# Performance work log

Measured on AMD Instinct MI355X. Metric: run time of the kernel, lower is better.

The kernel has to match this reference:

```python
import jax, jax.numpy as jnp
import numpy as np
from jax import lax

EPS = 1e-5
IC = 32  # inter_channels

def bn(x, g, b, m, v):
    sh = (1, -1, 1, 1)
    return (x - m.reshape(sh)) * (g.reshape(sh) * lax.rsqrt(v.reshape(sh) + EPS)) + b.reshape(sh)

def prelu(x, a):
    return jnp.where(x >= 0, x, a * x)

def conv1x1(x, w):  # x: [B,C,H,W], w: [O,C]
    return jnp.einsum('bchw,oc->bohw', x, w)

def dconv(x, w, d):  # 3x3 dilated conv, same padding
    return lax.conv_general_dilated(x, w, (1, 1), [(d, d), (d, d)], rhs_dilation=(d, d),
                                    dimension_numbers=('NCHW', 'OIHW', 'NCHW'))

def glca_forward(feature, q_w, q_gamma, q_beta, q_mean, q_var, q_alpha,
                 k_w, k_gamma, k_beta, k_mean, k_var, k_alpha,
                 v_w, v_gamma, v_beta, v_mean, v_var, v_alpha,
                 d1_w, d1_gamma, d1_beta, d1_mean, d1_var,
                 d2_w, d2_gamma, d2_beta, d2_mean, d2_var,
                 d3_w, d3_gamma, d3_beta, d3_mean, d3_var,
                 o_w, o_gamma, o_beta, o_mean, o_var, o_alpha):
    B, C, H, W = feature.shape
    q = prelu(bn(conv1x1(feature, q_w), q_gamma, q_beta, q_mean, q_var), q_alpha)  # [B,IC,H,W]
    k = prelu(bn(conv1x1(feature, k_w), k_gamma, k_beta, k_mean, k_var), k_alpha)
    val = prelu(bn(conv1x1(feature, v_w), v_gamma, v_beta, v_mean, v_var), v_alpha)
    qr = q.transpose(0, 3, 2, 1).reshape(B * W, H, IC)   # [BW,H,IC]
    kr = k.transpose(0, 3, 1, 2).reshape(B * W, IC, H)   # [BW,IC,H]
    att = jax.nn.softmax(jnp.matmul(qr, kr), axis=-1)    # [BW,H,H]
    branches = []
    for w, g, b, m, var, d in ((d1_w, d1_gamma, d1_beta, d1_mean, d1_var, 1),
                               (d2_w, d2_gamma, d2_beta, d2_mean, d2_var, 3),
                               (d3_w, d3_gamma, d3_beta, d3_mean, d3_var, 5)):
        t = jax.nn.relu(bn(dconv(val, w, d), g, b, m, var))          # [B,IC,H,W]
        # faithful to source: permute(0,3,1,2) then raw view to [BW,H,IC]
        t = t.transpose(0, 3, 1, 2).reshape(B * W, H, IC)
        branches.append(jnp.matmul(att, t))                          # [BW,H,IC]
    # faithful to source: cat along dim 0, then raw view(B,W,H,-1)
    res = jnp.concatenate(branches, axis=0).reshape(B, W, H, 3 * IC)
    res = res.transpose(0, 3, 2, 1)                                  # [B,3*IC,H,W]
    out = prelu(bn(conv1x1(res, o_w), o_gamma, o_beta, o_mean, o_var) + feature, o_alpha)
    return out

def setup_inputs() -> dict:
    B, C, H, W = 8, 256, 160, 160
    key = jax.random.key(0)
    ks = iter(jax.random.split(key, 48))
    d = {}
    d['feature'] = jax.random.normal(next(ks), (B, C, H, W), jnp.float32)
    for p in ('q', 'k', 'v'):
        d[p + '_w'] = jax.random.normal(next(ks), (IC, C), jnp.float32) * 0.05
        d[p + '_gamma'] = jax.random.uniform(next(ks), (IC,), jnp.float32, 0.5, 1.5)
        d[p + '_beta'] = jax.random.normal(next(ks), (IC,), jnp.float32) * 0.1
        d[p + '_mean'] = jax.random.normal(next(ks), (IC,), jnp.float32) * 0.1
        d[p + '_var'] = jax.random.uniform(next(ks), (IC,), jnp.float32, 0.5, 1.5)
        d[p + '_alpha'] = jnp.full((1,), 0.25, jnp.float32)
    for p in ('d1', 'd2', 'd3'):
        d[p + '_w'] = jax.random.normal(next(ks), (IC, IC, 3, 3), jnp.float32) * 0.05
        d[p + '_gamma'] = jax.random.uniform(next(ks), (IC,), jnp.float32, 0.5, 1.5)
        d[p + '_beta'] = jax.random.normal(next(ks), (IC,), jnp.float32) * 0.1
        d[p + '_mean'] = jax.random.normal(next(ks), (IC,), jnp.float32) * 0.1
        d[p + '_var'] = jax.random.uniform(next(ks), (IC,), jnp.float32, 0.5, 1.5)
    d['o_w'] = jax.random.normal(next(ks), (C, 3 * IC), jnp.float32) * 0.05
    d['o_gamma'] = jax.random.uniform(next(ks), (C,), jnp.float32, 0.5, 1.5)
    d['o_beta'] = jax.random.normal(next(ks), (C,), jnp.float32) * 0.1
    d['o_mean'] = jax.random.normal(next(ks), (C,), jnp.float32) * 0.1
    d['o_var'] = jax.random.uniform(next(ks), (C,), jnp.float32, 0.5, 1.5)
    d['o_alpha'] = jnp.full((1,), 0.25, jnp.float32)
    return d

def reference(feature, q_w, q_gamma, q_beta, q_mean, q_var, q_alpha,
              k_w, k_gamma, k_beta, k_mean, k_var, k_alpha,
              v_w, v_gamma, v_beta, v_mean, v_var, v_alpha,
              d1_w, d1_gamma, d1_beta, d1_mean, d1_var,
              d2_w, d2_gamma, d2_beta, d2_mean, d2_var,
              d3_w, d3_gamma, d3_beta, d3_mean, d3_var,
              o_w, o_gamma, o_beta, o_mean, o_var, o_alpha):
    return glca_forward(feature, q_w, q_gamma, q_beta, q_mean, q_var, q_alpha,
                        k_w, k_gamma, k_beta, k_mean, k_var, k_alpha,
                        v_w, v_gamma, v_beta, v_mean, v_var, v_alpha,
                        d1_w, d1_gamma, d1_beta, d1_mean, d1_var,
                        d2_w, d2_gamma, d2_beta, d2_mean, d2_var,
                        d3_w, d3_gamma, d3_beta, d3_mean, d3_var,
                        o_w, o_gamma, o_beta, o_mean, o_var, o_alpha)
```

## Files before the change

kernel.cpp:

```cpp
#include <hip/hip_runtime.h>

constexpr int Hh = 160, Ww = 160, Bb = 8, Cc = 256, ICn = 32;
constexpr int HWn = Hh * Ww;
constexpr float EPSf = 1e-5f;

constexpr int P_WQH  = 0;
constexpr int P_WQL  = 12288;
constexpr int P_QKVB = 24576;
constexpr int P_QKVA = 24672;
constexpr int P_DWB  = 24768;
constexpr int P_DB   = 52416;
constexpr int P_OWB  = 52512;
constexpr int P_OB   = 77088;
constexpr int P_OA   = 77344;
constexpr int PLANE  = Bb * ICn * HWn;
constexpr int OFF_Q  = 77824;
constexpr int OFF_K  = OFF_Q + PLANE;
constexpr int OFF_V  = OFF_Q + 2 * PLANE;
constexpr int OFF_T  = OFF_Q + 3 * PLANE;
constexpr int OFF_TPF= OFF_T + (3 * PLANE) / 2;
constexpr int OFF_CAT= OFF_Q + 6 * PLANE;

typedef unsigned short u16;
typedef short bf16x8 __attribute__((ext_vector_type(8)));
typedef float f32x4  __attribute__((ext_vector_type(4)));

__device__ __forceinline__ unsigned f2b(float x) {
    unsigned u = __float_as_uint(x);
    return (u + 0x7FFFu + ((u >> 16) & 1u)) >> 16;
}
__device__ __forceinline__ float b2f(unsigned b) { return __uint_as_float(b << 16); }

struct InPtrs { const float* p[40]; };

__global__ void k_prep(InPtrs in, float* __restrict__ ws) {
    int idx = blockIdx.x * 256 + threadIdx.x;
    if (idx < 24576) {
        int oc = idx >> 8, c = idx & 255;
        int z = oc >> 5, o = oc & 31;
        const float* wz = in.p[1 + 6 * z];
        float s = in.p[2 + 6 * z][o] * rsqrtf(in.p[5 + 6 * z][o] + EPSf);
        float wf = wz[o * 256 + c] * s;
        unsigned hi = f2b(wf);
        unsigned lo = f2b(wf - b2f(hi));
        ((u16*)(ws + P_WQH))[oc * 256 + c] = (u16)hi;
        ((u16*)(ws + P_WQL))[oc * 256 + c] = (u16)lo;
    } else if (idx < 24672) {
        int oc = idx - 24576; int z = oc >> 5, o = oc & 31;
        float s = in.p[2 + 6 * z][o] * rsqrtf(in.p[5 + 6 * z][o] + EPSf);
        ws[P_QKVB + oc] = in.p[3 + 6 * z][o] - in.p[4 + 6 * z][o] * s;
    } else if (idx < 24768) {
        int oc = idx - 24672; int z = oc >> 5;
        ws[P_QKVA + oc] = in.p[6 + 6 * z][0];
    } else if (idx < 52416) {
        int j = idx - 24768;
        int d = j / 9216, r2 = j % 9216;
        int oc = r2 & 31; int tmp = r2 >> 5;
        int kx = tmp % 3; tmp /= 3; int ky = tmp % 3; int ic2 = tmp / 3;
        const float* wd = in.p[19 + 5 * d];
        float s = in.p[20 + 5 * d][oc] * rsqrtf(in.p[23 + 5 * d][oc] + EPSf);
        float wf = wd[((oc * 32 + ic2) * 3 + ky) * 3 + kx] * s;
        ((u16*)(ws + P_DWB))[((d * 9 + ky * 3 + kx) * 32 + oc) * 32 + ic2] = (u16)f2b(wf);
    } else if (idx < 52512) {
        int j = idx - 52416; int d = j >> 5, oc = j & 31;
        float s = in.p[20 + 5 * d][oc] * rsqrtf(in.p[23 + 5 * d][oc] + EPSf);
        ws[P_DB + j] = in.p[21 + 5 * d][oc] - in.p[22 + 5 * d][oc] * s;
    } else if (idx < 77088) {
        int j2 = idx - 52512; int c = j2 / 96;
        float s = in.p[35][c] * rsqrtf(in.p[38][c] + EPSf);
        ((u16*)(ws + P_OWB))[j2] = (u16)f2b(in.p[34][j2] * s);
    } else if (idx < 77344) {
        int c = idx - 77088;
        float s = in.p[35][c] * rsqrtf(in.p[38][c] + EPSf);
        ws[P_OB + c] = in.p[36][c] - in.p[37][c] * s;
    } else if (idx == 77344) {
        ws[P_OA] = in.p[39][0];
    }
}

__global__ __launch_bounds__(64) void k_vpad(float* __restrict__ ws) {
    u16* Vt = (u16*)(ws + OFF_V);
    size_t base = (size_t)blockIdx.x * 176 * 32;
    int t = threadIdx.x;
    int off = (t < 32) ? t * 8 : (168 * 32 + (t - 32) * 8);
    uint4 z = {0u, 0u, 0u, 0u};
    *(uint4*)(Vt + base + off) = z;
}

__global__ __launch_bounds__(256) void k_qkv(const float* __restrict__ feat,
                                             float* __restrict__ ws) {
    __shared__ float FS[64 * 132];
    const int tid = threadIdx.x;
    const int wv = tid >> 6, l = tid & 63;
    const int g = l >> 4, c15 = l & 15;
    const int n0 = blockIdx.x * 128;
    const int b = n0 / HWn, hw0 = n0 % HWn;
    const float* fbase = feat + (size_t)b * Cc * HWn + hw0;
    const u16* __restrict__ WQH = (const u16*)(ws + P_WQH);
    const u16* __restrict__ WQL = (const u16*)(ws + P_WQL);

    f32x4 acc[6][2];
    f32x4 z4 = {0.f, 0.f, 0.f, 0.f};
#pragma unroll
    for (int mt = 0; mt < 6; mt++) { acc[mt][0] = z4; acc[mt][1] = z4; }

    for (int kc = 0; kc < 4; kc++) {
        __syncthreads();
#pragma unroll
        for (int i = 0; i < 8; i++) {
            int f = tid + i * 256;
            int row = f >> 5, col4 = f & 31;
            float4 v = *(const float4*)(fbase + (size_t)(kc * 64 + row) * HWn + col4 * 4);
            *(float4*)(&FS[row * 132 + col4 * 4]) = v;
        }
        __syncthreads();
#pragma unroll
        for (int ks = 0; ks < 2; ks++) {
            bf16x8 bh[2], bl[2];
#pragma unroll
            for (int ntl = 0; ntl < 2; ntl++) {
                int pos = (wv * 2 + ntl) * 16 + c15;
                unsigned hw_[4], lw_[4];
#pragma unroll
                for (int v2 = 0; v2 < 4; v2++) {
                    float x0 = FS[(ks * 32 + g * 8 + 2 * v2) * 132 + pos];
                    float x1 = FS[(ks * 32 + g * 8 + 2 * v2 + 1) * 132 + pos];
                    unsigned h0 = f2b(x0), h1 = f2b(x1);
                    unsigned l0 = f2b(x0 - b2f(h0)), l1 = f2b(x1 - b2f(h1));
                    hw_[v2] = h0 | (h1 << 16);
                    lw_[v2] = l0 | (l1 << 16);
                }
                uint4 hv = {hw_[0], hw_[1], hw_[2], hw_[3]};
                uint4 lv = {lw_[0], lw_[1], lw_[2], lw_[3]};
                bh[ntl] = *(bf16x8*)&hv;
                bl[ntl] = *(bf16x8*)&lv;
            }
#pragma unroll
            for (int mt = 0; mt < 6; mt++) {
                int arow = (16 * mt + c15) * 256 + kc * 64 + ks * 32 + g * 8;
                bf16x8 ah = *(const bf16x8*)(WQH + arow);
                bf16x8 al = *(const bf16x8*)(WQL + arow);
#pragma unroll
                for (int ntl = 0; ntl < 2; ntl++) {
                    acc[mt][ntl] = __builtin_amdgcn_mfma_f32_16x16x32_bf16(ah, bh[ntl], acc[mt][ntl], 0, 0, 0);
                    acc[mt][ntl] = __builtin_amdgcn_mfma_f32_16x16x32_bf16(ah, bl[ntl], acc[mt][ntl], 0, 0, 0);
                    acc[mt][ntl] = __builtin_amdgcn_mfma_f32_16x16x32_bf16(al, bh[ntl], acc[mt][ntl], 0, 0, 0);
                }
            }
        }
    }

    u16* vt = (u16*)(ws + OFF_V);
#pragma unroll
    for (int mt = 0; mt < 6; mt++)
#pragma unroll
        for (int ntl = 0; ntl < 2; ntl++) {
            int pos = hw0 + (wv * 2 + ntl) * 16 + c15;
            if (mt < 4) {
#pragma unroll
                for (int jr = 0; jr < 4; jr++) {
                    int oc = 16 * mt + 4 * g + jr;
                    float bb = ws[P_QKVB + oc];
                    float aa = ws[P_QKVA + oc];
                    float y = acc[mt][ntl][jr] + bb;
                    y = y >= 0.f ? y : aa * y;
                    int z = oc >> 5, o = oc & 31;
                    ws[OFF_Q + (size_t)z * PLANE + ((size_t)b * ICn + o) * HWn + pos] = y;
                }
            } else {
                int h = pos / 160, w2 = pos % 160;
                unsigned r[2];
#pragma unroll
                for (int p = 0; p < 2; p++) {
                    int oc = 16 * mt + 4 * g + 2 * p;
                    float y0 = acc[mt][ntl][2 * p]     + ws[P_QKVB + oc];
                    float y1 = acc[mt][ntl][2 * p + 1] + ws[P_QKVB + oc + 1];
                    float a0 = ws[P_QKVA + oc], a1 = ws[P_QKVA + oc + 1];
                    y0 = y0 >= 0.f ? y0 : a0 * y0;
                    y1 = y1 >= 0.f ? y1 : a1 * y1;
                    r[p] = f2b(y0) | (f2b(y1) << 16);
                }
                size_t a = ((size_t)(b * 160 + h) * 176 + w2 + 8) * 32 + (mt - 4) * 16 + 4 * g;
                uint2 dd; dd.x = r[0]; dd.y = r[1];
                *(uint2*)(vt + a) = dd;
            }
        }
}

__global__ __launch_bounds__(256) void k_dconv(float* __restrict__ ws) {
    const int tid = threadIdx.x;
    const int wv = tid >> 6, l = tid & 63;
    const int g = l >> 4, c15 = l & 15;
    const int b = blockIdx.y;
    const int d = blockIdx.z;
    const int dil = 1 + 2 * d;
    const int h0 = blockIdx.x * 2;
    const u16* __restrict__ WB = (const u16*)(ws + P_DWB) + d * 9 * 32 * 32;
    bf16x8 wb[9][2];
#pragma unroll
    for (int tap = 0; tap < 9; tap++)
#pragma unroll
        for (int n = 0; n < 2; n++)
            wb[tap][n] = *(const bf16x8*)(WB + ((size_t)tap * 32 + n * 16 + c15) * 32 + g * 8);
    const u16* __restrict__ Vt = (const u16*)(ws + OFF_V) + (size_t)b * 160 * 176 * 32;
    const float bias0 = ws[P_DB + d * 32 + c15];
    const float bias1 = ws[P_DB + d * 32 + 16 + c15];
    u16* __restrict__ tp = (u16*)(ws + OFF_TPF) + (size_t)(d * Bb + b) * ICn * HWn;
    f32x4 z4 = {0.f, 0.f, 0.f, 0.f};

    for (int t5 = 0; t5 < 5; t5++) {
        int t = wv * 5 + t5;
        int h = h0 + (t >= 10);
        int w0 = (t % 10) * 16;
        f32x4 acc0 = z4, acc1 = z4;
#pragma unroll
        for (int ky = 0; ky < 3; ky++) {
            int hh = h + dil * (ky - 1);
            if ((unsigned)hh >= 160u) continue;
            const u16* row = Vt + (size_t)hh * 176 * 32;
#pragma unroll
            for (int kx = 0; kx < 3; kx++) {
                int wbase = w0 + dil * (kx - 1) + 8;
                bf16x8 av = *(const bf16x8*)(row + (size_t)(wbase + c15) * 32 + g * 8);
                acc0 = __builtin_amdgcn_mfma_f32_16x16x32_bf16(av, wb[ky * 3 + kx][0], acc0, 0, 0, 0);
                acc1 = __builtin_amdgcn_mfma_f32_16x16x32_bf16(av, wb[ky * 3 + kx][1], acc1, 0, 0, 0);
            }
        }
        size_t pixb = (size_t)h * 160 + w0 + 4 * g;
        uint2 o0, o1;
        o0.x = f2b(fmaxf(acc0[0] + bias0, 0.f)) | (f2b(fmaxf(acc0[1] + bias0, 0.f)) << 16);
        o0.y = f2b(fmaxf(acc0[2] + bias0, 0.f)) | (f2b(fmaxf(acc0[3] + bias0, 0.f)) << 16);
        o1.x = f2b(fmaxf(acc1[0] + bias1, 0.f)) | (f2b(fmaxf(acc1[1] + bias1, 0.f)) << 16);
        o1.y = f2b(fmaxf(acc1[2] + bias1, 0.f)) | (f2b(fmaxf(acc1[3] + bias1, 0.f)) << 16);
        *(uint2*)(tp + (size_t)c15 * HWn + pixb) = o0;
        *(uint2*)(tp + (size_t)(16 + c15) * HWn + pixb) = o1;
    }
}

__global__ __launch_bounds__(256) void k_tfrag(float* __restrict__ ws) {
    __shared__ u16 fr[4][5120];
    const int tid = threadIdx.x;
    const int wq = blockIdx.x;
    const int b  = blockIdx.y;
    const int d  = blockIdx.z;
    const int w0 = wq * 4;
    const u16* __restrict__ tp = (const u16*)(ws + OFF_TPF) + (size_t)(d * Bb + b) * ICn * HWn;
    for (int i = tid; i < 5120; i += 256) {
        int ic = i / 160, h = i % 160;
        uint2 v = *(const uint2*)(tp + (size_t)ic * HWn + h * Ww + w0);
        fr[0][i] = (u16)(v.x & 0xFFFFu);
        fr[1][i] = (u16)(v.x >> 16);
        fr[2][i] = (u16)(v.y & 0xFFFFu);
        fr[3][i] = (u16)(v.y >> 16);
    }
    __syncthreads();
    u16* __restrict__ tf = (u16*)(ws + OFF_T);
#pragma unroll
    for (int it = 0; it < 10; it++) {
        int W = tid + it * 256;
        int s = W / 640, word = W % 640;
        int slot = word >> 6, lane = word & 63;
        int jc = (lane & 15) | ((slot / 5) << 4);
        int h2b = ((slot % 5) << 5) | (((lane >> 4) & 3) << 3);
        unsigned r[4];
#pragma unroll
        for (int p = 0; p < 4; p++) {
            int f0 = (h2b + 2 * p) * 32 + jc;
            unsigned lo = fr[s][f0];
            unsigned hi = fr[s][f0 + 32];
            r[p] = lo | (hi << 16);
        }
        uint4 o4 = {r[0], r[1], r[2], r[3]};
        *(uint4*)(tf + ((size_t)d * 1280 + b * 160 + w0 + s) * 5120 + word * 8) = o4;
    }
}

__global__ __launch_bounds__(256) void k_qkfrag(float* __restrict__ ws) {
    extern __shared__ float frf[];
    const int tid = threadIdx.x;
    const int wq = blockIdx.x;
    const int b  = blockIdx.y;
    const int z  = blockIdx.z;
    const int w0 = wq * 4;
    const float* __restrict__ in = ws + (z ? OFF_K : OFF_Q) + (size_t)b * ICn * HWn;
    u16* __restrict__ outb = (u16*)(ws + (z ? OFF_TPF : OFF_V));

    for (int i = tid; i < 5120; i += 256) {
        int ic = i / 160, h = i % 160;
        float4 v = *(const float4*)(in + (size_t)ic * HWn + h * 160 + w0);
        frf[0 * 5120 + i] = v.x;
        frf[1 * 5120 + i] = v.y;
        frf[2 * 5120 + i] = v.z;
        frf[3 * 5120 + i] = v.w;
    }
    __syncthreads();
#pragma unroll
    for (int it = 0; it < 10; it++) {
        int W = tid + it * 256;
        int s = W / 640, word = W % 640;
        int lane = word & 63, tau = word >> 6;
        int h = tau * 16 + (lane & 15);
        int icb = (lane >> 4) * 8;
        unsigned hw_[4], lw_[4];
#pragma unroll
        for (int p = 0; p < 4; p++) {
            float x0 = frf[s * 5120 + (icb + 2 * p) * 160 + h];
            float x1 = frf[s * 5120 + (icb + 2 * p + 1) * 160 + h];
            unsigned h0 = f2b(x0), h1 = f2b(x1);
            unsigned l0 = f2b(x0 - b2f(h0)), l1 = f2b(x1 - b2f(h1));
            hw_[p] = h0 | (h1 << 16);
            lw_[p] = l0 | (l1 << 16);
        }
        uint4 hv = {hw_[0], hw_[1], hw_[2], hw_[3]};
        uint4 lv = {lw_[0], lw_[1], lw_[2], lw_[3]};
        size_t o = (size_t)(b * 160 + w0 + s) * 5120 + word * 8;
        *(uint4*)(outb + o) = hv;
        *(uint4*)(outb + (size_t)PLANE + o) = lv;
    }
}

__global__ __launch_bounds__(320) void k_att(float* __restrict__ ws) {
    __shared__ char Sb[51200];
    const int tid = threadIdx.x;
    const int bid = blockIdx.x;
    const int r8 = bid & 7, qq = bid >> 3;
    const int b = qq / 20;
    const int w = r8 * 20 + (qq % 20);
    const int bw = b * Ww + w;
    const int wv = tid >> 6;
    const int l  = tid & 63;
    const int g  = l >> 4;
    const int c  = l & 15;
    const int slice = b * 160 + w;

    const u16* __restrict__ qh = (const u16*)(ws + OFF_V)   + (size_t)slice * 5120;
    const u16* __restrict__ ql = qh + (size_t)PLANE;
    const u16* __restrict__ kh = (const u16*)(ws + OFF_TPF) + (size_t)slice * 5120;
    const u16* __restrict__ kl = kh + (size_t)PLANE;

    bf16x8 bq[2][2];
#pragma unroll
    for (int ct = 0; ct < 2; ct++) {
        int tau = 2 * wv + ct;
        bq[ct][0] = *(const bf16x8*)(qh + (tau * 64 + l) * 8);
        bq[ct][1] = *(const bf16x8*)(ql + (tau * 64 + l) * 8);
    }
    f32x4 acc[10][2];
    f32x4 z4 = {0.f, 0.f, 0.f, 0.f};
#pragma unroll
    for (int rt = 0; rt < 10; rt++) { acc[rt][0] = z4; acc[rt][1] = z4; }
#pragma unroll
    for (int rt = 0; rt < 10; rt++) {
        bf16x8 ah = *(const bf16x8*)(kh + (rt * 64 + l) * 8);
        bf16x8 al = *(const bf16x8*)(kl + (rt * 64 + l) * 8);
#pragma unroll
        for (int ct = 0; ct < 2; ct++) {
            acc[rt][ct] = __builtin_amdgcn_mfma_f32_16x16x32_bf16(ah, bq[ct][0], acc[rt][ct], 0, 0, 0);
            acc[rt][ct] = __builtin_amdgcn_mfma_f32_16x16x32_bf16(ah, bq[ct][1], acc[rt][ct], 0, 0, 0);
            acc[rt][ct] = __builtin_amdgcn_mfma_f32_16x16x32_bf16(al, bq[ct][0], acc[rt][ct], 0, 0, 0);
        }
    }

    float mx[2] = {-3.4e38f, -3.4e38f};
#pragma unroll
    for (int rt = 0; rt < 10; rt++)
#pragma unroll
        for (int ct = 0; ct < 2; ct++)
#pragma unroll
            for (int j = 0; j < 4; j++) mx[ct] = fmaxf(mx[ct], acc[rt][ct][j]);
#pragma unroll
    for (int ct = 0; ct < 2; ct++) {
        mx[ct] = fmaxf(mx[ct], __shfl_xor(mx[ct], 16));
        mx[ct] = fmaxf(mx[ct], __shfl_xor(mx[ct], 32));
    }
    float sm[2] = {0.f, 0.f};
#pragma unroll
    for (int rt = 0; rt < 10; rt++)
#pragma unroll
        for (int ct = 0; ct < 2; ct++)
#pragma unroll
            for (int j = 0; j < 4; j++) {
                float e = __expf(acc[rt][ct][j] - mx[ct]);
                acc[rt][ct][j] = e;
                sm[ct] += e;
            }
#pragma unroll
    for (int ct = 0; ct < 2; ct++) {
        sm[ct] += __shfl_xor(sm[ct], 16);
        sm[ct] += __shfl_xor(sm[ct], 32);
    }
    float inv[2] = {1.f / sm[0], 1.f / sm[1]};

#pragma unroll
    for (int rt = 0; rt < 10; rt++) {
#pragma unroll
        for (int ct = 0; ct < 2; ct++) {
            float p0 = acc[rt][ct][0] * inv[ct];
            float p1 = acc[rt][ct][1] * inv[ct];
            float p2 = acc[rt][ct][2] * inv[ct];
            float p3 = acc[rt][ct][3] * inv[ct];
            unsigned d0 = f2b(p0) | (f2b(p1) << 16);
            unsigned d1 = f2b(p2) | (f2b(p3) << 16);
            int Lf = c + 16 * (2 * (rt & 1) + (g >> 1));
            char* dst = Sb + (((wv * 2 + ct) * 5 + (rt >> 1)) * 64 + Lf) * 16 + 8 * (g & 1);
            uint2 dd; dd.x = d0; dd.y = d1;
            *(uint2*)dst = dd;
        }
    }

    const u16* tf = (const u16*)(ws + OFF_T);
    u16* catb = (u16*)(ws + OFF_CAT);
    for (int d = 0; d < 3; d++) {
        const u16* tfd = tf + ((size_t)d * (Bb * Ww) + bw) * 5120;
        f32x4 po[2][2];
        po[0][0] = z4; po[0][1] = z4; po[1][0] = z4; po[1][1] = z4;
#pragma unroll
        for (int ks = 0; ks < 5; ks++) {
            bf16x8 a0 = *(const bf16x8*)(tfd + ((0 * 5 + ks) * 64 + l) * 8);
            bf16x8 a1 = *(const bf16x8*)(tfd + ((1 * 5 + ks) * 64 + l) * 8);
            bf16x8 s0 = *(bf16x8*)(Sb + (((wv * 2 + 0) * 5 + ks) * 64 + l) * 16);
            bf16x8 s1 = *(bf16x8*)(Sb + (((wv * 2 + 1) * 5 + ks) * 64 + l) * 16);
            po[0][0] = __builtin_amdgcn_mfma_f32_16x16x32_bf16(a0, s0, po[0][0], 0, 0, 0);
            po[0][1] = __builtin_amdgcn_mfma_f32_16x16x32_bf16(a0, s1, po[0][1], 0, 0, 0);
            po[1][0] = __builtin_amdgcn_mfma_f32_16x16x32_bf16(a1, s0, po[1][0], 0, 0, 0);
            po[1][1] = __builtin_amdgcn_mfma_f32_16x16x32_bf16(a1, s1, po[1][1], 0, 0, 0);
        }
#pragma unroll
        for (int jt = 0; jt < 2; jt++)
#pragma unroll
            for (int ct = 0; ct < 2; ct++) {
                int h1 = 32 * wv + 16 * ct + c;
                size_t idx = (size_t)d * PLANE + (size_t)bw * 5120 + h1 * 32 + 16 * jt + 4 * g;
                f32x4 v = po[jt][ct];
                uint2 dd;
                dd.x = f2b(v[0]) | (f2b(v[1]) << 16);
                dd.y = f2b(v[2]) | (f2b(v[3]) << 16);
                *(uint2*)(catb + idx) = dd;
            }
    }
}

__global__ __launch_bounds__(256) void k_out(const float* __restrict__ feat,
                                             const float* __restrict__ ws,
                                             float* __restrict__ out) {
    __shared__ u16 Bs[12288];
    const int tid = threadIdx.x;
    const int wv = tid >> 6, l = tid & 63;
    const int g = l >> 4, c15 = l & 15;
    const int n0 = blockIdx.x * 128;
    const int b = n0 / HWn, hw0 = n0 % HWn;
    const u16* __restrict__ CATb = (const u16*)(ws + OFF_CAT);
    const u16* __restrict__ OWB = (const u16*)(ws + P_OWB);

#pragma unroll
    for (int ss = 0; ss < 6; ss++) {
        int s = tid + ss * 256;
        int sl = s & 63, si = s >> 6;
        int p = (si & 7) * 16 + (sl & 15);
        int hw = hw0 + p;
        int h = hw / Ww, w2 = hw % Ww;
        int j = (si >> 3) * 32 + (sl >> 4) * 8;
        size_t flat = ((size_t)(b * Ww + w2) * Hh + h) * 96 + j;
        *(uint4*)(&Bs[(si * 64 + sl) * 8]) = *(const uint4*)(CATb + flat);
    }
    bf16x8 af[4][3];
#pragma unroll
    for (int mt = 0; mt < 4; mt++)
#pragma unroll
        for (int ks = 0; ks < 3; ks++)
            af[mt][ks] = *(const bf16x8*)(OWB + (wv * 64 + mt * 16 + c15) * 96 + ks * 32 + g * 8);
    __syncthreads();
    const float alpha = ws[P_OA];

    f32x4 z4 = {0.f, 0.f, 0.f, 0.f};
#pragma unroll
    for (int np = 0; np < 2; np++) {
        f32x4 acc[4][4];
#pragma unroll
        for (int mt = 0; mt < 4; mt++)
#pragma unroll
            for (int ntl = 0; ntl < 4; ntl++) acc[mt][ntl] = z4;
#pragma unroll
        for (int ks = 0; ks < 3; ks++) {
            bf16x8 bf_[4];
#pragma unroll
            for (int ntl = 0; ntl < 4; ntl++)
                bf_[ntl] = *(const bf16x8*)(&Bs[((ks * 8 + np * 4 + ntl) * 64 + l) * 8]);
#pragma unroll
            for (int mt = 0; mt < 4; mt++)
#pragma unroll
                for (int ntl = 0; ntl < 4; ntl++)
                    acc[mt][ntl] = __builtin_amdgcn_mfma_f32_16x16x32_bf16(af[mt][ks], bf_[ntl], acc[mt][ntl], 0, 0, 0);
        }
#pragma unroll
        for (int mt = 0; mt < 4; mt++)
#pragma unroll
            for (int ntl = 0; ntl < 4; ntl++) {
                int p = (np * 4 + ntl) * 16 + c15;
#pragma unroll
                for (int jr = 0; jr < 4; jr++) {
                    int cch = wv * 64 + mt * 16 + 4 * g + jr;
                    size_t base = ((size_t)b * Cc + cch) * HWn + hw0 + p;
                    float y = acc[mt][ntl][jr] + ws[P_OB + cch] + feat[base];
                    out[base] = y >= 0.f ? y : alpha * y;
                }
            }
    }
}

extern "C" void kernel_launch(void* const* d_in, const int* in_sizes, int n_in,
                              void* d_out, int out_size, void* d_ws, size_t ws_size,
                              hipStream_t stream) {
    InPtrs ip;
    for (int i = 0; i < 40; i++) ip.p[i] = (const float*)d_in[i];
    float* ws = (float*)d_ws;
    const float* feat = (const float*)d_in[0];
    float* out = (float*)d_out;

    k_prep<<<304, 256, 0, stream>>>(ip, ws);
    k_vpad<<<1280, 64, 0, stream>>>(ws);
    k_qkv<<<1600, 256, 0, stream>>>(feat, ws);
    k_dconv<<<dim3(80, 8, 3), 256, 0, stream>>>(ws);
    k_tfrag<<<dim3(40, 8, 3), 256, 0, stream>>>(ws);
    (void)hipFuncSetAttribute(reinterpret_cast<const void*>(k_qkfrag),
                              hipFuncAttributeMaxDynamicSharedMemorySize, 81920);
    k_qkfrag<<<dim3(40, 8, 2), 256, 81920, stream>>>(ws);
    k_att<<<1280, 320, 0, stream>>>(ws);
    k_out<<<1600, 256, 0, stream>>>(feat, ws, out);
}
```

Before: 471.2 us.

## Pipeline k_qkv feature loads with async global-to-LDS four-stage ring buffer

Replaces the synchronous register-staged load of feature tiles in the QKV projection kernel with direct global-to-LDS async loads into a 4-deep ring of 32-channel slices, gated by explicit vmcnt waits and barriers. Loads for later chunks are issued while MFMA work runs on earlier ones, to hide global memory latency. LDS use grows to 64 KB of dynamic shared memory, which may lower occupancy. The LDS row padding is removed, so bank conflicts on reads may rise.

```diff
diff --git a/kernel.cpp b/kernel.cpp
--- a/kernel.cpp
+++ b/kernel.cpp
@@ -30,6 +30,10 @@
     return (u + 0x7FFFu + ((u >> 16) & 1u)) >> 16;
 }
 __device__ __forceinline__ float b2f(unsigned b) { return __uint_as_float(b << 16); }
+
+#define GLOAD_LDS16(gp, lp) __builtin_amdgcn_global_load_lds( \
+    (const __attribute__((address_space(1))) void*)(gp), \
+    (__attribute__((address_space(3))) void*)(lp), 16, 0, 0)
 
 struct InPtrs { const float* p[40]; };
 
@@ -89,7 +93,7 @@
 
 __global__ __launch_bounds__(256) void k_qkv(const float* __restrict__ feat,
                                              float* __restrict__ ws) {
-    __shared__ float FS[64 * 132];
+    extern __shared__ float FSs[];
     const int tid = threadIdx.x;
     const int wv = tid >> 6, l = tid & 63;
     const int g = l >> 4, c15 = l & 15;
@@ -104,49 +108,63 @@
 #pragma unroll
     for (int mt = 0; mt < 6; mt++) { acc[mt][0] = z4; acc[mt][1] = z4; }
 
+#pragma unroll
     for (int kc = 0; kc < 4; kc++) {
-        __syncthreads();
-#pragma unroll
-        for (int i = 0; i < 8; i++) {
-            int f = tid + i * 256;
-            int row = f >> 5, col4 = f & 31;
-            float4 v = *(const float4*)(fbase + (size_t)(kc * 64 + row) * HWn + col4 * 4);
-            *(float4*)(&FS[row * 132 + col4 * 4]) = v;
-        }
-        __syncthreads();
-#pragma unroll
-        for (int ks = 0; ks < 2; ks++) {
-            bf16x8 bh[2], bl[2];
+        float* dst = FSs + kc * 4096 + wv * 1024;
+        const float* src = fbase + (size_t)(kc * 32 + wv * 8) * HWn;
+#pragma unroll
+        for (int j = 0; j < 4; j++)
+            GLOAD_LDS16(src + (size_t)(2 * j + (l >> 5)) * HWn + (l & 31) * 4, dst + j * 256);
+    }
+
+#pragma unroll
+    for (int kc = 0; kc < 8; kc++) {
+        if (kc <= 4)      asm volatile("s_waitcnt vmcnt(12)" ::: "memory");
+        else if (kc == 5) asm volatile("s_waitcnt vmcnt(8)" ::: "memory");
+        else if (kc == 6) asm volatile("s_waitcnt vmcnt(4)" ::: "memory");
+        else              asm volatile("s_waitcnt vmcnt(0)" ::: "memory");
+        __builtin_amdgcn_s_barrier();
+        asm volatile("" ::: "memory");
+        const float* B = FSs + (kc & 3) * 4096;
+        bf16x8 bh[2], bl[2];
+#pragma unroll
+        for (int ntl = 0; ntl < 2; ntl++) {
+            int pos = (wv * 2 + ntl) * 16 + c15;
+            unsigned hw_[4], lw_[4];
+#pragma unroll
+            for (int v2 = 0; v2 < 4; v2++) {
+                float x0 = B[(g * 8 + 2 * v2) * 128 + pos];
+                float x1 = B[(g * 8 + 2 * v2 + 1) * 128 + pos];
+                unsigned h0 = f2b(x0), h1 = f2b(x1);
+                unsigned l0 = f2b(x0 - b2f(h0)), l1 = f2b(x1 - b2f(h1));
+                hw_[v2] = h0 | (h1 << 16);
+                lw_[v2] = l0 | (l1 << 16);
+            }
+            uint4 hv = {hw_[0], hw_[1], hw_[2], hw_[3]};
+            uint4 lv = {lw_[0], lw_[1], lw_[2], lw_[3]};
+            bh[ntl] = *(bf16x8*)&hv;
+            bl[ntl] = *(bf16x8*)&lv;
+        }
+#pragma unroll
+        for (int mt = 0; mt < 6; mt++) {
+            int arow = (16 * mt + c15) * 256 + kc * 32 + g * 8;
+            bf16x8 ah = *(const bf16x8*)(WQH + arow);
+            bf16x8 al = *(const bf16x8*)(WQL + arow);
 #pragma unroll
             for (int ntl = 0; ntl < 2; ntl++) {
-                int pos = (wv * 2 + ntl) * 16 + c15;
-                unsigned hw_[4], lw_[4];
-#pragma unroll
-                for (int v2 = 0; v2 < 4; v2++) {
-                    float x0 = FS[(ks * 32 + g * 8 + 2 * v2) * 132 + pos];
-                    float x1 = FS[(ks * 32 + g * 8 + 2 * v2 + 1) * 132 + pos];
-                    unsigned h0 = f2b(x0), h1 = f2b(x1);
-                    unsigned l0 = f2b(x0 - b2f(h0)), l1 = f2b(x1 - b2f(h1));
-                    hw_[v2] = h0 | (h1 << 16);
-                    lw_[v2] = l0 | (l1 << 16);
-                }
-                uint4 hv = {hw_[0], hw_[1], hw_[2], hw_[3]};
-                uint4 lv = {lw_[0], lw_[1], lw_[2], lw_[3]};
-                bh[ntl] = *(bf16x8*)&hv;
-                bl[ntl] = *(bf16x8*)&lv;
-            }
-#pragma unroll
-            for (int mt = 0; mt < 6; mt++) {
-                int arow = (16 * mt + c15) * 256 + kc * 64 + ks * 32 + g * 8;
-                bf16x8 ah = *(const bf16x8*)(WQH + arow);
-                bf16x8 al = *(const bf16x8*)(WQL + arow);
-#pragma unroll
-                for (int ntl = 0; ntl < 2; ntl++) {
-                    acc[mt][ntl] = __builtin_amdgcn_mfma_f32_16x16x32_bf16(ah, bh[ntl], acc[mt][ntl], 0, 0, 0);
-                    acc[mt][ntl] = __builtin_amdgcn_mfma_f32_16x16x32_bf16(ah, bl[ntl], acc[mt][ntl], 0, 0, 0);
-                    acc[mt][ntl] = __builtin_amdgcn_mfma_f32_16x16x32_bf16(al, bh[ntl], acc[mt][ntl], 0, 0, 0);
-                }
-            }
+                acc[mt][ntl] = __builtin_amdgcn_mfma_f32_16x16x32_bf16(ah, bh[ntl], acc[mt][ntl], 0, 0, 0);
+                acc[mt][ntl] = __builtin_amdgcn_mfma_f32_16x16x32_bf16(ah, bl[ntl], acc[mt][ntl], 0, 0, 0);
+                acc[mt][ntl] = __builtin_amdgcn_mfma_f32_16x16x32_bf16(al, bh[ntl], acc[mt][ntl], 0, 0, 0);
+            }
+        }
+        __builtin_amdgcn_s_barrier();
+        asm volatile("" ::: "memory");
+        if (kc + 4 < 8) {
+            float* dst = FSs + (kc & 3) * 4096 + wv * 1024;
+            const float* src = fbase + (size_t)((kc + 4) * 32 + wv * 8) * HWn;
+#pragma unroll
+            for (int j = 0; j < 4; j++)
+                GLOAD_LDS16(src + (size_t)(2 * j + (l >> 5)) * HWn + (l & 31) * 4, dst + j * 256);
         }
     }
 
@@ -519,7 +537,9 @@
 
     k_prep<<<304, 256, 0, stream>>>(ip, ws);
     k_vpad<<<1280, 64, 0, stream>>>(ws);
-    k_qkv<<<1600, 256, 0, stream>>>(feat, ws);
+    (void)hipFuncSetAttribute(reinterpret_cast<const void*>(k_qkv),
+                              hipFuncAttributeMaxDynamicSharedMemorySize, 65536);
+    k_qkv<<<1600, 256, 65536, stream>>>(feat, ws);
     k_dconv<<<dim3(80, 8, 3), 256, 0, stream>>>(ws);
     k_tfrag<<<dim3(40, 8, 3), 256, 0, stream>>>(ws);
     (void)hipFuncSetAttribute(reinterpret_cast<const void*>(k_qkfrag),
```

Result: faster. 461.0 us (-2.2%).
